# Kernel optimization log

Hardware: AMD Instinct MI355X
Metric: run time of the kernel (lower is better)

The kernel has to match this reference:

```python
import jax, jax.numpy as jnp
import numpy as np

def setup_inputs() -> dict:
    key = jax.random.key(0)
    k1, k2 = jax.random.split(key)
    B, H, Q = 65536, 1024, 8
    hidden_state = jax.random.normal(k1, (B, H), dtype=jnp.float32)
    # nn.Linear(hidden_dim, n_qubits): weight [Q, H], bias [Q]
    W = jax.random.normal(k2, (Q, H), dtype=jnp.float32) * (1.0 / np.sqrt(H))
    b = jnp.zeros((Q,), dtype=jnp.float32)
    return {"hidden_state": hidden_state, "W": W, "b": b}

def reference(hidden_state, W, b):
    # Linear projection: [B, H] @ [H, Q] + [Q] -> [B, Q] (RX rotation angles)
    theta = jnp.einsum('bh,qh->bq', hidden_state, W) + b
    # RX(theta) on |0> gives P(|0>) = cos^2(theta/2) per qubit.
    # probs(all wires)[0] = P(|00..0>) = prod_i cos^2(theta_i/2)  (closed form,
    # equivalent to the full 2^n state-vector simulation in the original).
    c = jnp.cos(theta * 0.5)
    p0 = jnp.prod(c * c, axis=-1)  # [B]
    return jnp.mean(1.0 - p0)
```

## Files before the change

kernel.cpp:

```cpp
#include <hip/hip_runtime.h>


#define HDIM 1024
#define QN 8
#define RPB 64
#define CHUNK 256
#define ROUNDS 4
#define ROW_STRIDE 260

__global__ __launch_bounds__(1024, 8)
void qreg_kernel(const float* __restrict__ hidden,
                 const float* __restrict__ W,
                 const float* __restrict__ bias,
                 float* __restrict__ out) {
    __shared__ __align__(16) float tile[RPB * ROW_STRIDE];

    const int tid  = threadIdx.x;
    const int lane = tid & 63;
    const int w    = __builtin_amdgcn_readfirstlane(tid >> 6);
    const size_t row_base = (size_t)blockIdx.x * RPB;

    float acc[QN];
#pragma unroll
    for (int q = 0; q < QN; ++q) acc[q] = 0.f;

#pragma unroll
    for (int k = 0; k < ROUNDS; ++k) {
#pragma unroll
        for (int i = 0; i < 4; ++i) {
            const int r = 4 * w + i;
            const float* g = hidden + (row_base + r) * HDIM + k * CHUNK + lane * 4;
            __builtin_amdgcn_global_load_lds(
                (const __attribute__((address_space(1))) void*)g,
                (__attribute__((address_space(3))) void*)&tile[r * ROW_STRIDE],
                16, 0, 0);
        }
        __syncthreads();

        float4 x0 = *reinterpret_cast<const float4*>(&tile[lane * ROW_STRIDE + w * 16 + 0]);
        float4 x1 = *reinterpret_cast<const float4*>(&tile[lane * ROW_STRIDE + w * 16 + 4]);
        float4 x2 = *reinterpret_cast<const float4*>(&tile[lane * ROW_STRIDE + w * 16 + 8]);
        float4 x3 = *reinterpret_cast<const float4*>(&tile[lane * ROW_STRIDE + w * 16 + 12]);

        const float* wbase = W + k * CHUNK + w * 16;
#pragma unroll
        for (int q = 0; q < QN; ++q) {
            const float* wq = wbase + q * HDIM;
            acc[q] += x0.x * wq[0]  + x0.y * wq[1]  + x0.z * wq[2]  + x0.w * wq[3]
                    + x1.x * wq[4]  + x1.y * wq[5]  + x1.z * wq[6]  + x1.w * wq[7]
                    + x2.x * wq[8]  + x2.y * wq[9]  + x2.z * wq[10] + x2.w * wq[11]
                    + x3.x * wq[12] + x3.y * wq[13] + x3.z * wq[14] + x3.w * wq[15];
        }
        __syncthreads();
    }

    float* part = tile;
#pragma unroll
    for (int q = 0; q < QN; ++q)
        part[(w * RPB + lane) * 9 + q] = acc[q];
    __syncthreads();

    float* theta = tile + 9216;
    if (tid < 512) {
        const int r = tid >> 3, q = tid & 7;
        float th = bias[q];
#pragma unroll
        for (int ww = 0; ww < 16; ++ww)
            th += part[(ww * RPB + r) * 9 + q];
        theta[r * 8 + q] = th;
    }
    __syncthreads();

    if (tid < 64) {
        float p0 = 1.f;
#pragma unroll
        for (int q = 0; q < QN; ++q) {
            float c = __cosf(0.5f * theta[tid * 8 + q]);
            p0 *= c * c;
        }
        float contrib = 1.f - p0;
#pragma unroll
        for (int off = 32; off > 0; off >>= 1)
            contrib += __shfl_down(contrib, off);
        if (tid == 0)
            atomicAdd(out, contrib * (1.0f / 65536.0f));
    }
}

extern "C" void kernel_launch(void* const* d_in, const int* in_sizes, int n_in,
                              void* d_out, int out_size, void* d_ws, size_t ws_size,
                              hipStream_t stream) {
    const float* hidden = (const float*)d_in[0];
    const float* W      = (const float*)d_in[1];
    const float* bias   = (const float*)d_in[2];
    float* out          = (float*)d_out;

    hipMemsetAsync(out, 0, sizeof(float), stream);
    qreg_kernel<<<65536 / RPB, 1024, 0, stream>>>(hidden, W, bias, out);
}
```

Baseline: 364.1 us.

## Give each wave its own column segment with double-buffered async LDS loads

```diff
diff --git a/kernel.cpp b/kernel.cpp
--- a/kernel.cpp
+++ b/kernel.cpp
@@ -4,79 +4,99 @@
 #define HDIM 1024
 #define QN 8
 #define RPB 64
-#define CHUNK 256
-#define ROUNDS 4
-#define ROW_STRIDE 260
+#define SEG 256
+#define CHUNK 32
+#define NCHUNK 8
+#define INST_PAD 1040
+#define BUF_BYTES (8 * INST_PAD)
+#define WAVE_BYTES (2 * BUF_BYTES)
 
-__global__ __launch_bounds__(1024, 8)
+__global__ __launch_bounds__(256, 2)
 void qreg_kernel(const float* __restrict__ hidden,
                  const float* __restrict__ W,
                  const float* __restrict__ bias,
                  float* __restrict__ out) {
-    __shared__ __align__(16) float tile[RPB * ROW_STRIDE];
+    __shared__ __align__(16) char lds[4 * WAVE_BYTES];
 
     const int tid  = threadIdx.x;
     const int lane = tid & 63;
     const int w    = __builtin_amdgcn_readfirstlane(tid >> 6);
     const size_t row_base = (size_t)blockIdx.x * RPB;
 
+    const int r = lane & 7;
+    const int s = lane >> 3;
+
+    char* wlds = lds + w * WAVE_BYTES;
+    const float* gbase = hidden + (row_base + r) * HDIM + w * SEG + s * 4;
+
+#pragma unroll
+    for (int i = 0; i < 8; ++i) {
+        __builtin_amdgcn_global_load_lds(
+            (const __attribute__((address_space(1))) void*)(gbase + (size_t)(i * 8) * HDIM),
+            (__attribute__((address_space(3))) void*)(wlds + i * INST_PAD),
+            16, 0, 0);
+    }
+
     float acc[QN];
 #pragma unroll
     for (int q = 0; q < QN; ++q) acc[q] = 0.f;
 
 #pragma unroll
-    for (int k = 0; k < ROUNDS; ++k) {
+    for (int c = 0; c < NCHUNK; ++c) {
+        const int b = c & 1;
+
+        const char* rowb = wlds + b * BUF_BYTES + (lane >> 3) * INST_PAD + (lane & 7) * 16;
+        float4 x[8];
 #pragma unroll
-        for (int i = 0; i < 4; ++i) {
-            const int r = 4 * w + i;
-            const float* g = hidden + (row_base + r) * HDIM + k * CHUNK + lane * 4;
-            __builtin_amdgcn_global_load_lds(
-                (const __attribute__((address_space(1))) void*)g,
-                (__attribute__((address_space(3))) void*)&tile[r * ROW_STRIDE],
-                16, 0, 0);
+        for (int j = 0; j < 8; ++j)
+            x[j] = *reinterpret_cast<const float4*>(rowb + j * 128);
+
+        if (c + 1 < NCHUNK) {
+#pragma unroll
+            for (int i = 0; i < 8; ++i) {
+                __builtin_amdgcn_global_load_lds(
+                    (const __attribute__((address_space(1))) void*)(gbase + (size_t)(i * 8) * HDIM + (c + 1) * CHUNK),
+                    (__attribute__((address_space(3))) void*)(wlds + (b ^ 1) * BUF_BYTES + i * INST_PAD),
+                    16, 0, 0);
+            }
         }
-        __syncthreads();
 
-        float4 x0 = *reinterpret_cast<const float4*>(&tile[lane * ROW_STRIDE + w * 16 + 0]);
-        float4 x1 = *reinterpret_cast<const float4*>(&tile[lane * ROW_STRIDE + w * 16 + 4]);
-        float4 x2 = *reinterpret_cast<const float4*>(&tile[lane * ROW_STRIDE + w * 16 + 8]);
-        float4 x3 = *reinterpret_cast<const float4*>(&tile[lane * ROW_STRIDE + w * 16 + 12]);
-
-        const float* wbase = W + k * CHUNK + w * 16;
+        const float* wseg = W + w * SEG + c * CHUNK;
 #pragma unroll
         for (int q = 0; q < QN; ++q) {
-            const float* wq = wbase + q * HDIM;
-            acc[q] += x0.x * wq[0]  + x0.y * wq[1]  + x0.z * wq[2]  + x0.w * wq[3]
-                    + x1.x * wq[4]  + x1.y * wq[5]  + x1.z * wq[6]  + x1.w * wq[7]
-                    + x2.x * wq[8]  + x2.y * wq[9]  + x2.z * wq[10] + x2.w * wq[11]
-                    + x3.x * wq[12] + x3.y * wq[13] + x3.z * wq[14] + x3.w * wq[15];
+            const float* wq = wseg + q * HDIM;
+            float a = acc[q];
+#pragma unroll
+            for (int j = 0; j < 8; ++j) {
+                a += x[j].x * wq[j * 4 + 0] + x[j].y * wq[j * 4 + 1]
+                   + x[j].z * wq[j * 4 + 2] + x[j].w * wq[j * 4 + 3];
+            }
+            acc[q] = a;
         }
-        __syncthreads();
     }
 
-    float* part = tile;
+    __syncthreads();
+    float* part = (float*)lds;
 #pragma unroll
     for (int q = 0; q < QN; ++q)
-        part[(w * RPB + lane) * 9 + q] = acc[q];
-    __syncthreads();
-
-    float* theta = tile + 9216;
-    if (tid < 512) {
-        const int r = tid >> 3, q = tid & 7;
-        float th = bias[q];
-#pragma unroll
-        for (int ww = 0; ww < 16; ++ww)
-            th += part[(ww * RPB + r) * 9 + q];
-        theta[r * 8 + q] = th;
-    }
+        part[(w * RPB + lane) * 8 + q] = acc[q];
     __syncthreads();
 
     if (tid < 64) {
+        float th[QN];
+#pragma unroll
+        for (int q = 0; q < QN; ++q) th[q] = bias[q];
+#pragma unroll
+        for (int ww = 0; ww < 4; ++ww)
+#pragma unroll
+            for (int q = 0; q < QN; ++q)
+                th[q] += part[(ww * RPB + tid) * 8 + q];
+
         float p0 = 1.f;
 #pragma unroll
         for (int q = 0; q < QN; ++q) {
-            float c = __cosf(0.5f * theta[tid * 8 + q]);
-            p0 *= c * c;
+            float cc = __cosf(0.5f * th[q]);
+            p0 *= cc * cc;
         }
         float contrib = 1.f - p0;
 #pragma unroll
@@ -96,5 +116,5 @@
     float* out          = (float*)d_out;
 
     hipMemsetAsync(out, 0, sizeof(float), stream);
-    qreg_kernel<<<65536 / RPB, 1024, 0, stream>>>(hidden, W, bias, out);
+    qreg_kernel<<<65536 / RPB, 256, 0, stream>>>(hidden, W, bias, out);
 }
```

After: 391.5 us. +7.5%, slower.

## Process rows per wave with register-cached weights and shuffle reductions

Applied to the files above, without the earlier changes.

```diff
diff --git a/kernel.cpp b/kernel.cpp
--- a/kernel.cpp
+++ b/kernel.cpp
@@ -3,88 +3,79 @@
 
 #define HDIM 1024
 #define QN 8
-#define RPB 64
-#define CHUNK 256
-#define ROUNDS 4
-#define ROW_STRIDE 260
+#define RPW 16
 
-__global__ __launch_bounds__(1024, 8)
+__global__ __launch_bounds__(256, 2)
 void qreg_kernel(const float* __restrict__ hidden,
                  const float* __restrict__ W,
                  const float* __restrict__ bias,
                  float* __restrict__ out) {
-    __shared__ __align__(16) float tile[RPB * ROW_STRIDE];
-
     const int tid  = threadIdx.x;
     const int lane = tid & 63;
-    const int w    = __builtin_amdgcn_readfirstlane(tid >> 6);
-    const size_t row_base = (size_t)blockIdx.x * RPB;
+    const int wave = blockIdx.x * 4 + (tid >> 6);
+    const size_t row0 = (size_t)wave * RPW;
 
-    float acc[QN];
+    float4 wf[QN][4];
 #pragma unroll
-    for (int q = 0; q < QN; ++q) acc[q] = 0.f;
+    for (int q = 0; q < QN; ++q)
+#pragma unroll
+        for (int i = 0; i < 4; ++i)
+            wf[q][i] = *reinterpret_cast<const float4*>(W + q * HDIM + i * 256 + lane * 4);
+
+    float bi[QN];
+#pragma unroll
+    for (int q = 0; q < QN; ++q) bi[q] = bias[q];
+
+    const float* rp = hidden + row0 * HDIM + lane * 4;
+
+    float4 xbuf[3][4];
+#pragma unroll
+    for (int i = 0; i < 4; ++i) {
+        xbuf[0][i] = *reinterpret_cast<const float4*>(rp + 0 * HDIM + i * 256);
+        xbuf[1][i] = *reinterpret_cast<const float4*>(rp + 1 * HDIM + i * 256);
+    }
+
+    float bsum = 0.f;
 
 #pragma unroll
-    for (int k = 0; k < ROUNDS; ++k) {
+    for (int r = 0; r < RPW; ++r) {
+        const int cur = r % 3;
+        if (r + 2 < RPW) {
+            const int nxt = (r + 2) % 3;
 #pragma unroll
-        for (int i = 0; i < 4; ++i) {
-            const int r = 4 * w + i;
-            const float* g = hidden + (row_base + r) * HDIM + k * CHUNK + lane * 4;
-            __builtin_amdgcn_global_load_lds(
-                (const __attribute__((address_space(1))) void*)g,
-                (__attribute__((address_space(3))) void*)&tile[r * ROW_STRIDE],
-                16, 0, 0);
+            for (int i = 0; i < 4; ++i)
+                xbuf[nxt][i] = *reinterpret_cast<const float4*>(rp + (size_t)(r + 2) * HDIM + i * 256);
         }
-        __syncthreads();
 
-        float4 x0 = *reinterpret_cast<const float4*>(&tile[lane * ROW_STRIDE + w * 16 + 0]);
-        float4 x1 = *reinterpret_cast<const float4*>(&tile[lane * ROW_STRIDE + w * 16 + 4]);
-        float4 x2 = *reinterpret_cast<const float4*>(&tile[lane * ROW_STRIDE + w * 16 + 8]);
-        float4 x3 = *reinterpret_cast<const float4*>(&tile[lane * ROW_STRIDE + w * 16 + 12]);
-
-        const float* wbase = W + k * CHUNK + w * 16;
+        float t[QN];
 #pragma unroll
         for (int q = 0; q < QN; ++q) {
-            const float* wq = wbase + q * HDIM;
-            acc[q] += x0.x * wq[0]  + x0.y * wq[1]  + x0.z * wq[2]  + x0.w * wq[3]
-                    + x1.x * wq[4]  + x1.y * wq[5]  + x1.z * wq[6]  + x1.w * wq[7]
-                    + x2.x * wq[8]  + x2.y * wq[9]  + x2.z * wq[10] + x2.w * wq[11]
-                    + x3.x * wq[12] + x3.y * wq[13] + x3.z * wq[14] + x3.w * wq[15];
+            float a = 0.f;
+#pragma unroll
+            for (int i = 0; i < 4; ++i) {
+                a += xbuf[cur][i].x * wf[q][i].x + xbuf[cur][i].y * wf[q][i].y
+                   + xbuf[cur][i].z * wf[q][i].z + xbuf[cur][i].w * wf[q][i].w;
+            }
+            t[q] = a;
         }
-        __syncthreads();
-    }
 
-    float* part = tile;
 #pragma unroll
-    for (int q = 0; q < QN; ++q)
-        part[(w * RPB + lane) * 9 + q] = acc[q];
-    __syncthreads();
+        for (int off = 1; off < 64; off <<= 1)
+#pragma unroll
+            for (int q = 0; q < QN; ++q)
+                t[q] += __shfl_xor(t[q], off, 64);
 
-    float* theta = tile + 9216;
-    if (tid < 512) {
-        const int r = tid >> 3, q = tid & 7;
-        float th = bias[q];
-#pragma unroll
-        for (int ww = 0; ww < 16; ++ww)
-            th += part[(ww * RPB + r) * 9 + q];
-        theta[r * 8 + q] = th;
-    }
-    __syncthreads();
-
-    if (tid < 64) {
         float p0 = 1.f;
 #pragma unroll
         for (int q = 0; q < QN; ++q) {
-            float c = __cosf(0.5f * theta[tid * 8 + q]);
+            float c = __cosf(0.5f * (t[q] + bi[q]));
             p0 *= c * c;
         }
-        float contrib = 1.f - p0;
-#pragma unroll
-        for (int off = 32; off > 0; off >>= 1)
-            contrib += __shfl_down(contrib, off);
-        if (tid == 0)
-            atomicAdd(out, contrib * (1.0f / 65536.0f));
+        bsum += 1.f - p0;
     }
+
+    if (lane == 0)
+        atomicAdd(out, bsum * (1.0f / 65536.0f));
 }
 
 extern "C" void kernel_launch(void* const* d_in, const int* in_sizes, int n_in,
@@ -96,5 +87,5 @@
     float* out          = (float*)d_out;
 
     hipMemsetAsync(out, 0, sizeof(float), stream);
-    qreg_kernel<<<65536 / RPB, 1024, 0, stream>>>(hidden, W, bias, out);
+    qreg_kernel<<<1024, 256, 0, stream>>>(hidden, W, bias, out);
 }
```

Result: slower. 453.7 us (+24.6%).
